# Performance work log

Hardware: AMD Instinct MI355X
Metric: run time of the kernel (lower is better)

Reference implementation:

```python
import jax, jax.numpy as jnp
import numpy as np


def setup_inputs() -> dict:
    key = jax.random.key(0)
    k1, k2, k3 = jax.random.split(key, 3)
    B, C, E = 65536, 32, 512
    candidate_ids = jax.random.randint(k1, (B, C), 0, E, dtype=jnp.int64)
    candidate_scores = jax.random.uniform(k2, (B, C), dtype=jnp.float32)
    cooc = jax.random.uniform(k3, (E, E), dtype=jnp.float32)
    # row-normalize like update_cooccurrence would maintain
    cooc = cooc / jnp.clip(cooc.sum(axis=1, keepdims=True), 1e-8)
    return {
        "candidate_ids": candidate_ids,
        "candidate_scores": candidate_scores,
        "cooccurrence": cooc,
        "target_size": 64,
    }


def reference(candidate_ids, candidate_scores, cooccurrence, target_size):
    B, C = candidate_ids.shape
    E = cooccurrence.shape[0]
    num_to_add = target_size - C  # static; original returns early if <= 0
    rows = jnp.arange(B)[:, None]  # [B,1]
    # sum_i score[b,i] * cooccurrence[ids[b,i]]  ==  scatter scores into [B,E], then matmul
    sparse_scores = jnp.zeros((B, E), jnp.float32).at[rows, candidate_ids].add(candidate_scores)
    cooc_scores = sparse_scores @ cooccurrence  # [B,E]
    # mask out existing candidates
    cooc_scores = cooc_scores.at[rows, candidate_ids].set(-jnp.inf)
    additional_scores, additional_ids = jax.lax.top_k(cooc_scores, num_to_add)
    expanded_ids = jnp.concatenate([candidate_ids, additional_ids.astype(candidate_ids.dtype)], axis=-1)
    expanded_scores = jnp.concatenate([candidate_scores, additional_scores], axis=-1)
    return expanded_ids, expanded_scores
```

## Files before the change

kernel.cpp:

```cpp
#include <hip/hip_runtime.h>
#include <stdint.h>

typedef unsigned long long u64;
typedef unsigned int u32;
typedef float vf2 __attribute__((ext_vector_type(2)));

constexpr int Ccand = 32;
constexpr int Evoc  = 512;
constexpr int Tgt   = 64;

template<int J>
__device__ __forceinline__ int shx32(int x) {
    if constexpr (J == 1)       return __builtin_amdgcn_update_dpp(0, x, 0xB1, 0xF, 0xF, true);
    else if constexpr (J == 2)  return __builtin_amdgcn_update_dpp(0, x, 0x4E, 0xF, 0xF, true);
    else if constexpr (J <= 16) return __builtin_amdgcn_ds_swizzle(x, (J << 10) | 0x1F);
    else                        return __shfl_xor(x, J);
}

template<int K2, int J>
__device__ __forceinline__ void cas_f32(float& a, int lane) {
    float o = __int_as_float(shx32<J>(__float_as_int(a)));
    bool keepMax = (((lane & K2) == 0) == ((lane & J) == 0));
    bool g = a > o;
    a = (keepMax == g) ? a : o;
}

template<int K2, int J>
__device__ __forceinline__ void cas_u64(u64& a, int lane) {
    int lo = shx32<J>((int)(u32)a);
    int hi = shx32<J>((int)(u32)(a >> 32));
    u64 o = ((u64)(u32)hi << 32) | (u32)lo;
    bool keepMax = (((lane & K2) == 0) == ((lane & J) == 0));
    bool g = a > o;
    a = (keepMax == g) ? a : o;
}

__device__ __forceinline__ void sort64_desc_f32(float& a, int lane) {
    cas_f32<2,1>(a,lane);
    cas_f32<4,2>(a,lane);   cas_f32<4,1>(a,lane);
    cas_f32<8,4>(a,lane);   cas_f32<8,2>(a,lane);   cas_f32<8,1>(a,lane);
    cas_f32<16,8>(a,lane);  cas_f32<16,4>(a,lane);  cas_f32<16,2>(a,lane);  cas_f32<16,1>(a,lane);
    cas_f32<32,16>(a,lane); cas_f32<32,8>(a,lane);  cas_f32<32,4>(a,lane);  cas_f32<32,2>(a,lane);  cas_f32<32,1>(a,lane);
    cas_f32<64,32>(a,lane); cas_f32<64,16>(a,lane); cas_f32<64,8>(a,lane);  cas_f32<64,4>(a,lane);  cas_f32<64,2>(a,lane); cas_f32<64,1>(a,lane);
}

__device__ __forceinline__ void sort64_desc_u64(u64& a, int lane) {
    cas_u64<2,1>(a,lane);
    cas_u64<4,2>(a,lane);   cas_u64<4,1>(a,lane);
    cas_u64<8,4>(a,lane);   cas_u64<8,2>(a,lane);   cas_u64<8,1>(a,lane);
    cas_u64<16,8>(a,lane);  cas_u64<16,4>(a,lane);  cas_u64<16,2>(a,lane);  cas_u64<16,1>(a,lane);
    cas_u64<32,16>(a,lane); cas_u64<32,8>(a,lane);  cas_u64<32,4>(a,lane);  cas_u64<32,2>(a,lane);  cas_u64<32,1>(a,lane);
    cas_u64<64,32>(a,lane); cas_u64<64,16>(a,lane); cas_u64<64,8>(a,lane);  cas_u64<64,4>(a,lane);  cas_u64<64,2>(a,lane); cas_u64<64,1>(a,lane);
}

__device__ __forceinline__ u32 rev16(u32 x) {
    return __builtin_bitreverse32(x) >> 16;
}

__global__ __launch_bounds__(256, 8) void cooc_expand(
    const int* __restrict__ cand_ids,
    const float* __restrict__ cand_scores,
    const float* __restrict__ cooc,
    float* __restrict__ out_ids,
    float* __restrict__ out_scores,
    int B)
{
    const int lane = threadIdx.x & 63;
    const int wid  = threadIdx.x >> 6;
    const int row  = blockIdx.x * 4 + wid;
    __shared__ u64 buf[4][64];
    __shared__ u32 maskw[4][16];
    if (row >= B) return;

    if (lane < 16) maskw[wid][lane] = 0u;
    int   my_id = -1;
    float my_s  = 0.0f;
    if (lane < Ccand) {
        my_id = cand_ids[(size_t)row * Ccand + lane];
        my_s  = cand_scores[(size_t)row * Ccand + lane];
    }
    __threadfence_block();
    if (lane < Ccand)
        atomicOr(&maskw[wid][(u32)my_id >> 5], 1u << (my_id & 31));

    int pid = __shfl_xor(my_id, 32);
    int qid = (lane < 32) ? my_id : pid;
    const int jb4 = (lane < 32) ? 0 : (16 << 2);
    u32 acc_eq = 0u, acc_lt = 0u;
    #pragma unroll
    for (int t = 0; t < 16; ++t) {
        int idj = __builtin_amdgcn_ds_bpermute(jb4 + (t << 2), my_id);
        acc_eq = (acc_eq << 1) | (idj == qid ? 1u : 0u);
        acc_lt = (acc_lt << 1) | (idj <  qid ? 1u : 0u);
    }
    u32 pk = (rev16(acc_eq) << 16) | rev16(acc_lt);
    u32 op = (u32)__shfl_xor((int)pk, 32);
    u32 eqm = (pk >> 16) | (op & 0xFFFF0000u);
    u32 ltm = (pk & 0xFFFFu) | (op << 16);

    u32 below = (1u << (lane & 31)) - 1u;
    bool alive = (lane < Ccand) && ((eqm & below) == 0u);
    u64 aball = __ballot(alive);
    int m  = __popcll(aball);
    int rk = __popc(ltm & (u32)aball);

    float smv = my_s;
    u32 rem = alive ? (eqm & ~(1u << (lane & 31))) : 0u;
    while (__any(rem != 0u)) {
        int j = __ffs(rem) - 1;
        float sj = __int_as_float(__builtin_amdgcn_ds_bpermute(j << 2, __float_as_int(my_s)));
        smv += (rem != 0u) ? sj : 0.0f;
        rem &= rem - 1u;
    }

    int dst = alive ? rk : ((lane < 32) ? (lane + 32) : lane);
    int sorted_id = __builtin_amdgcn_ds_permute(dst << 2, my_id);
    int sorted_sb = __builtin_amdgcn_ds_permute(dst << 2, __float_as_int(smv));

    vf2 acc2[4];
    acc2[0] = (vf2){0.f, 0.f}; acc2[1] = (vf2){0.f, 0.f};
    acc2[2] = (vf2){0.f, 0.f}; acc2[3] = (vf2){0.f, 0.f};
    const int l4 = lane << 2;
    #pragma unroll 1
    for (int t = 0; t < m; t += 4) {
        int   e[4];
        float s[4];
        #pragma unroll
        for (int u = 0; u < 4; ++u) {
            int idx  = t + u;
            int idxc = (idx < m) ? idx : (m - 1);
            e[u] = __builtin_amdgcn_readlane(sorted_id, idxc) & 511;
            s[u] = (idx < m) ? __int_as_float(__builtin_amdgcn_readlane(sorted_sb, idx)) : 0.0f;
        }
        float4 A[4], Bv[4];
        #pragma unroll
        for (int u = 0; u < 4; ++u) {
            const float* rp = cooc + ((size_t)e[u] << 9);
            A[u]  = *reinterpret_cast<const float4*>(rp + l4);
            Bv[u] = *reinterpret_cast<const float4*>(rp + 256 + l4);
        }
        #pragma unroll
        for (int u = 0; u < 4; ++u) {
            vf2 sv2; sv2[0] = s[u]; sv2[1] = s[u];
            vf2 a0; a0[0] = A[u].x;  a0[1] = A[u].y;
            vf2 a1; a1[0] = A[u].z;  a1[1] = A[u].w;
            vf2 b0; b0[0] = Bv[u].x; b0[1] = Bv[u].y;
            vf2 b1; b1[0] = Bv[u].z; b1[1] = Bv[u].w;
            acc2[0] = __builtin_elementwise_fma(sv2, a0, acc2[0]);
            acc2[1] = __builtin_elementwise_fma(sv2, a1, acc2[1]);
            acc2[2] = __builtin_elementwise_fma(sv2, b0, acc2[2]);
            acc2[3] = __builtin_elementwise_fma(sv2, b1, acc2[3]);
        }
    }

    __threadfence_block();
    u32 wA = maskw[wid][lane >> 3];
    u32 wB = maskw[wid][8 + (lane >> 3)];
    int sh = (lane & 7) << 2;
    u32 mb = ((wA >> sh) & 15u) | (((wB >> sh) & 15u) << 4);

    float v[8];
    v[0] = acc2[0][0]; v[1] = acc2[0][1]; v[2] = acc2[1][0]; v[3] = acc2[1][1];
    v[4] = acc2[2][0]; v[5] = acc2[2][1]; v[6] = acc2[3][0]; v[7] = acc2[3][1];
    #pragma unroll
    for (int j = 0; j < 8; ++j)
        if ((mb >> j) & 1u) v[j] = -1.0f;

    float mx8 = v[0];
    #pragma unroll
    for (int j = 1; j < 8; ++j) mx8 = fmaxf(mx8, v[j]);
    float srt = mx8;
    sort64_desc_f32(srt, lane);
    float L32 = __int_as_float(__builtin_amdgcn_readlane(__float_as_int(srt), 31));

    int cnt = 0;
    #pragma unroll
    for (int j = 0; j < 8; ++j) cnt += (v[j] >= L32) ? 1 : 0;
    int sbase = 0, S_tot = 0;
    #pragma unroll
    for (int b = 0; b < 4; ++b) {
        u64 bal = __ballot(((cnt >> b) & 1) != 0);
        int pc = __builtin_amdgcn_mbcnt_hi((u32)(bal >> 32),
                 __builtin_amdgcn_mbcnt_lo((u32)bal, 0));
        sbase += pc << b;
        S_tot += ((int)__popcll(bal)) << b;
    }

    int nchunk = (S_tot + 63) >> 6;
    u64 cur = 0ull;
    #pragma unroll 1
    for (int c = 0; c < nchunk; ++c) {
        const int lo = c << 6;
        int slot = sbase;
        #pragma unroll
        for (int j = 0; j < 8; ++j) {
            bool s = (v[j] >= L32);
            int  rel = slot - lo;
            if (s && rel >= 0 && rel < 64) {
                int col = (j < 4) ? (l4 + j) : (256 + l4 + (j - 4));
                buf[wid][rel] = ((u64)__float_as_uint(v[j]) << 32) | (u32)(511 - col);
            }
            slot += s ? 1 : 0;
        }
        __threadfence_block();
        u64 nxt = (lo + lane < S_tot) ? buf[wid][lane] : 0ull;
        __threadfence_block();
        sort64_desc_u64(nxt, lane);
        if (c == 0) {
            cur = nxt;
        } else {
            u64 o = __shfl_xor(nxt, 63);
            cur = (cur >= o) ? cur : o;
            cas_u64<64,32>(cur, lane);
            cas_u64<64,16>(cur, lane);
            cas_u64<64,8>(cur, lane);
            cas_u64<64,4>(cur, lane);
            cas_u64<64,2>(cur, lane);
            cas_u64<64,1>(cur, lane);
        }
    }

    int src = (lane >= 32) ? (lane - 32) : 0;
    u64 kk = __shfl(cur, src);
    const size_t ob = (size_t)row * Tgt;
    float oid, osc;
    if (lane < Ccand) {
        oid = (float)my_id;
        osc = my_s;
    } else {
        oid = (float)(int)(511 - (u32)(kk & 511ull));
        osc = __uint_as_float((u32)(kk >> 32));
    }
    out_ids[ob + lane]    = oid;
    out_scores[ob + lane] = osc;
}

extern "C" void kernel_launch(void* const* d_in, const int* in_sizes, int n_in,
                              void* d_out, int out_size, void* d_ws, size_t ws_size,
                              hipStream_t stream) {
    const int*   ids    = (const int*)d_in[0];
    const float* scores = (const float*)d_in[1];
    const float* cooc   = (const float*)d_in[2];
    int B = in_sizes[0] / Ccand;
    float* out_ids    = (float*)d_out;
    float* out_scores = out_ids + (size_t)B * Tgt;
    int blocks = (B + 3) / 4;
    hipLaunchKernelGGL(cooc_expand, dim3(blocks), dim3(256), 0, stream,
                       ids, scores, cooc, out_ids, out_scores, B);
}
```

Measured before the change: 203.7 us.

## Software-pipeline cooccurrence row loads with double-buffered inline asm loads

Replaces the 4-row-per-iteration gather loop with a ping-pong double-buffered loop that processes two rows per step. The loads for the next pair are issued before the current pair is accumulated, using inline-asm global loads and explicit vmcnt waits. The aim is to hide global/L2 load latency behind the FMAs instead of stalling on each batch of loads. In exchange, inline asm with manual waitcnt and sched barriers bypasses the compiler's own scheduling. Any other outstanding vector-memory ops would also break the vmcnt(4) assumption.

New measurement: 203.5 us. No clear change (-0.1%).

```diff
diff --git a/kernel.cpp b/kernel.cpp
--- a/kernel.cpp
+++ b/kernel.cpp
@@ -55,6 +55,21 @@
 
 __device__ __forceinline__ u32 rev16(u32 x) {
     return __builtin_bitreverse32(x) >> 16;
+}
+
+__device__ __forceinline__ void gload2(const float* p, float4& lo, float4& hi) {
+    asm volatile("global_load_dwordx4 %0, %2, off\n\t"
+                 "global_load_dwordx4 %1, %2, off offset:1024"
+                 : "=&v"(lo), "=&v"(hi)
+                 : "v"(p));
+}
+__device__ __forceinline__ void wait_vm4() {
+    asm volatile("s_waitcnt vmcnt(4)" ::);
+    __builtin_amdgcn_sched_barrier(0);
+}
+__device__ __forceinline__ void wait_vm0() {
+    asm volatile("s_waitcnt vmcnt(0)" ::);
+    __builtin_amdgcn_sched_barrier(0);
 }
 
 __global__ __launch_bounds__(256, 8) void cooc_expand(
@@ -121,36 +136,69 @@
     acc2[0] = (vf2){0.f, 0.f}; acc2[1] = (vf2){0.f, 0.f};
     acc2[2] = (vf2){0.f, 0.f}; acc2[3] = (vf2){0.f, 0.f};
     const int l4 = lane << 2;
-    #pragma unroll 1
-    for (int t = 0; t < m; t += 4) {
-        int   e[4];
-        float s[4];
-        #pragma unroll
-        for (int u = 0; u < 4; ++u) {
-            int idx  = t + u;
-            int idxc = (idx < m) ? idx : (m - 1);
-            e[u] = __builtin_amdgcn_readlane(sorted_id, idxc) & 511;
-            s[u] = (idx < m) ? __int_as_float(__builtin_amdgcn_readlane(sorted_sb, idx)) : 0.0f;
-        }
-        float4 A[4], Bv[4];
-        #pragma unroll
-        for (int u = 0; u < 4; ++u) {
-            const float* rp = cooc + ((size_t)e[u] << 9);
-            A[u]  = *reinterpret_cast<const float4*>(rp + l4);
-            Bv[u] = *reinterpret_cast<const float4*>(rp + 256 + l4);
-        }
-        #pragma unroll
-        for (int u = 0; u < 4; ++u) {
-            vf2 sv2; sv2[0] = s[u]; sv2[1] = s[u];
-            vf2 a0; a0[0] = A[u].x;  a0[1] = A[u].y;
-            vf2 a1; a1[0] = A[u].z;  a1[1] = A[u].w;
-            vf2 b0; b0[0] = Bv[u].x; b0[1] = Bv[u].y;
-            vf2 b1; b1[0] = Bv[u].z; b1[1] = Bv[u].w;
-            acc2[0] = __builtin_elementwise_fma(sv2, a0, acc2[0]);
-            acc2[1] = __builtin_elementwise_fma(sv2, a1, acc2[1]);
-            acc2[2] = __builtin_elementwise_fma(sv2, b0, acc2[2]);
-            acc2[3] = __builtin_elementwise_fma(sv2, b1, acc2[3]);
-        }
+    const int mm1 = m - 1;
+    const float* lbase = cooc + l4;
+
+    auto fma8 = [&](float sv0, const float4& lo0, const float4& hi0,
+                    float sv1, const float4& lo1, const float4& hi1) {
+        vf2 s_, x_;
+        s_[0] = sv0; s_[1] = sv0;
+        x_[0] = lo0.x; x_[1] = lo0.y; acc2[0] = __builtin_elementwise_fma(s_, x_, acc2[0]);
+        x_[0] = lo0.z; x_[1] = lo0.w; acc2[1] = __builtin_elementwise_fma(s_, x_, acc2[1]);
+        x_[0] = hi0.x; x_[1] = hi0.y; acc2[2] = __builtin_elementwise_fma(s_, x_, acc2[2]);
+        x_[0] = hi0.z; x_[1] = hi0.w; acc2[3] = __builtin_elementwise_fma(s_, x_, acc2[3]);
+        s_[0] = sv1; s_[1] = sv1;
+        x_[0] = lo1.x; x_[1] = lo1.y; acc2[0] = __builtin_elementwise_fma(s_, x_, acc2[0]);
+        x_[0] = lo1.z; x_[1] = lo1.w; acc2[1] = __builtin_elementwise_fma(s_, x_, acc2[1]);
+        x_[0] = hi1.x; x_[1] = hi1.y; acc2[2] = __builtin_elementwise_fma(s_, x_, acc2[2]);
+        x_[0] = hi1.z; x_[1] = hi1.w; acc2[3] = __builtin_elementwise_fma(s_, x_, acc2[3]);
+    };
+
+    float4 A0, A1, A2, A3, B0, B1, B2, B3;
+    {
+        int pj  = (1 <= mm1) ? 1 : mm1;
+        int e0  = __builtin_amdgcn_readlane(sorted_id, 0) & 511;
+        int e1  = __builtin_amdgcn_readlane(sorted_id, pj) & 511;
+        gload2(lbase + ((size_t)e0 << 9), A0, A1);
+        gload2(lbase + ((size_t)e1 << 9), A2, A3);
+    }
+    float sA0 = __int_as_float(__builtin_amdgcn_readlane(sorted_sb, 0));
+    float sA1 = (1 < m) ? __int_as_float(__builtin_amdgcn_readlane(sorted_sb, (1 <= mm1) ? 1 : mm1)) : 0.0f;
+    float sB0 = 0.0f, sB1 = 0.0f;
+    int t = 0;
+    for (;;) {
+        bool pf = (t + 2 < m);
+        if (pf) {
+            int q1 = (t + 3 <= mm1) ? (t + 3) : mm1;
+            int f0 = __builtin_amdgcn_readlane(sorted_id, t + 2) & 511;
+            int f1 = __builtin_amdgcn_readlane(sorted_id, q1) & 511;
+            sB0 = __int_as_float(__builtin_amdgcn_readlane(sorted_sb, t + 2));
+            sB1 = (t + 3 < m) ? __int_as_float(__builtin_amdgcn_readlane(sorted_sb, q1)) : 0.0f;
+            gload2(lbase + ((size_t)f0 << 9), B0, B1);
+            gload2(lbase + ((size_t)f1 << 9), B2, B3);
+            wait_vm4();
+        } else {
+            wait_vm0();
+        }
+        fma8(sA0, A0, A1, sA1, A2, A3);
+        if (!pf) break;
+        t += 2;
+        pf = (t + 2 < m);
+        if (pf) {
+            int q1 = (t + 3 <= mm1) ? (t + 3) : mm1;
+            int f0 = __builtin_amdgcn_readlane(sorted_id, t + 2) & 511;
+            int f1 = __builtin_amdgcn_readlane(sorted_id, q1) & 511;
+            sA0 = __int_as_float(__builtin_amdgcn_readlane(sorted_sb, t + 2));
+            sA1 = (t + 3 < m) ? __int_as_float(__builtin_amdgcn_readlane(sorted_sb, q1)) : 0.0f;
+            gload2(lbase + ((size_t)f0 << 9), A0, A1);
+            gload2(lbase + ((size_t)f1 << 9), A2, A3);
+            wait_vm4();
+        } else {
+            wait_vm0();
+        }
+        fma8(sB0, B0, B1, sB1, B2, B3);
+        if (!pf) break;
+        t += 2;
     }
 
     __threadfence_block();
```
